# Optimization experiments

Measured on AMD Instinct MI355X. Metric: run time of the kernel, lower is better.

Reference implementation:

```python
import jax, jax.numpy as jnp
import numpy as np

B, D, OUT, K = 2048, 256, 256, 16


def setup_inputs() -> dict:
    key = jax.random.key(0)
    k1, k2, k3, k4 = jax.random.split(key, 4)
    x = jax.random.normal(k1, (B, D), dtype=jnp.float32)
    values = jax.random.uniform(k2, (OUT, D, K), dtype=jnp.float32, minval=-0.05, maxval=0.05)
    skip_w = jax.random.normal(k3, (OUT, D), dtype=jnp.float32) * (1.0 / np.sqrt(D).astype(np.float32))
    skip_b = jax.random.normal(k4, (OUT,), dtype=jnp.float32) * 0.01
    return {"x": x, "values": values, "skip_w": skip_w, "skip_b": skip_b}


def reference(x, values, skip_w, skip_b):
    # x: (B, D); values: (OUT, D, K); skip_w: (OUT, D); skip_b: (OUT,)
    num_knots = values.shape[-1]
    grid = jnp.linspace(-1.0, 1.0, num_knots)  # (K,)
    xc = jnp.clip(x, -1.0, 1.0)
    # torch.bucketize(x, grid) with right=False == searchsorted side='left'
    right = jnp.searchsorted(grid, xc, side='left')
    left = jnp.clip(right - 1, 0, num_knots - 2)  # (B, D)
    right = left + 1
    g0 = grid[left]
    g1 = grid[right]
    w = (xc - g0) / (g1 - g0 + 1e-12)  # (B, D)
    # Gather spline values per (sample, input-dim) knot bucket.
    vt = jnp.transpose(values, (1, 2, 0))  # (D, K, OUT)
    dim_idx = jnp.arange(xc.shape[1])[None, :]  # (1, D)
    v_left = vt[dim_idx, left]    # (B, D, OUT)
    v_right = vt[dim_idx, right]  # (B, D, OUT)
    # Linear interpolation + sum over input dims.
    y = jnp.sum((1.0 - w)[..., None] * v_left + w[..., None] * v_right, axis=1)  # (B, OUT)
    # Skip connection on the clamped input (torch reassigns x = clamp(x) first).
    return y + xc @ skip_w.T + skip_b
```

## Files before the change

kernel.cpp:

```cpp
#include <hip/hip_runtime.h>
#include <hip/hip_bf16.h>


namespace {
constexpr int Bsz  = 2048;
constexpr int Din  = 256;
constexpr int Dout = 256;
constexpr int Kn   = 16;
constexpr int KKNOT = Din * Kn;
constexpr int Ksp   = KKNOT + Din;
constexpr float INV_H = 7.5f;
constexpr float Hgrid = 2.0f / 15.0f;

constexpr int BM = 64, BN = 64, BK = 64;
constexpr int TOTSTEP = Ksp / BK;
constexpr int NSPLIT  = 4;
constexpr int STEPS   = TOTSTEP / NSPLIT;
constexpr int MT = Bsz / BM;
constexpr int NT = Dout / BN;
}

typedef __attribute__((ext_vector_type(8))) short shortx8;
typedef __attribute__((ext_vector_type(4))) float floatx4;
typedef __attribute__((address_space(3))) unsigned int lds_u32;
typedef __attribute__((address_space(1))) const unsigned int gbl_u32;

__device__ __forceinline__ unsigned int f2bf(float f) {
  __hip_bfloat16 h = __float2bfloat16(f);
  return (unsigned int)*reinterpret_cast<unsigned short*>(&h);
}

__global__ __launch_bounds__(256) void build_wt(
    const float* __restrict__ values, const float* __restrict__ skip_w,
    unsigned short* __restrict__ Wt) {
  const int c = blockIdx.x * 256 + threadIdx.x;
  const float* src;
  unsigned short* dst;
  if (c < KKNOT * Dout / 8) {
    const int o = c >> 9, i = c & 511;
    src = values + (size_t)c * 8;
    dst = Wt + (size_t)o * Ksp + i * 8;
  } else {
    const int c2 = c - KKNOT * Dout / 8;
    const int o = c2 >> 5, i = c2 & 31;
    src = skip_w + (size_t)c2 * 8;
    dst = Wt + (size_t)o * Ksp + KKNOT + i * 8;
  }
  const float4 v0 = *(const float4*)src;
  const float4 v1 = *(const float4*)(src + 4);
  *(uint4*)dst = make_uint4(f2bf(v0.x) | (f2bf(v0.y) << 16),
                            f2bf(v0.z) | (f2bf(v0.w) << 16),
                            f2bf(v1.x) | (f2bf(v1.y) << 16),
                            f2bf(v1.z) | (f2bf(v1.w) << 16));
}

__global__ __launch_bounds__(256) void kan_gemm(
    const float* __restrict__ x, const unsigned short* __restrict__ Wt,
    float* __restrict__ part) {
  __shared__ __align__(16) unsigned short As[BM][BK];
  __shared__ __align__(16) unsigned short Bs[BN][BK];

  const int tid = threadIdx.x;
  const int ks  = blockIdx.x % NSPLIT;
  const int nt  = (blockIdx.x / NSPLIT) % NT;
  const int mt  = blockIdx.x / (NSPLIT * NT);
  const int m0 = mt * BM, n0 = nt * BN;
  const int g0 = ks * STEPS, g1 = g0 + STEPS;

  const int row = tid >> 2;
  const int q   = tid & 3;
  const int b   = m0 + row;

  const int wave = tid >> 6, lane = tid & 63;
  const int wm = (wave & 1) * 32, wn = (wave >> 1) * 32;
  const int lrow = lane & 15, lq = lane >> 4;

  floatx4 acc[2][2] = {};

  for (int g = g0; g < g1; ++g) {
    __syncthreads();

    #pragma unroll
    for (int p = 0; p < 2; ++p) {
      const int c = tid + p * 256;
      const int n = c >> 3, kcs = c & 7;
      const int kc = kcs ^ (n & 7);
      const unsigned short* gsrc = Wt + (size_t)(n0 + n) * Ksp + g * 64 + kc * 8;
      unsigned int* l = (unsigned int*)(&Bs[0][0]) + c * 4;
      __builtin_amdgcn_global_load_lds((gbl_u32*)gsrc, (lds_u32*)l, 16, 0, 0);
    }

    unsigned int u[8];
    if (g < KKNOT / BK) {
      const float xr = x[(size_t)b * Din + 4 * g + q];
      const float t = (fminf(1.f, fmaxf(-1.f, xr)) + 1.f) * INV_H;
      #pragma unroll
      for (int i = 0; i < 8; ++i) {
        const float a0 = fmaxf(0.f, 1.f - fabsf(t - (float)(2 * i)));
        const float a1 = fmaxf(0.f, 1.f - fabsf(t - (float)(2 * i + 1)));
        u[i] = f2bf(a0) | (f2bf(a1) << 16);
      }
    } else {
      const int off = (g - KKNOT / BK) * 64 + q * 16;
      const float4* xq = (const float4*)(x + (size_t)b * Din + off);
      #pragma unroll
      for (int p = 0; p < 4; ++p) {
        const float4 v = xq[p];
        u[2 * p]     = f2bf(fminf(1.f, fmaxf(-1.f, v.x))) | (f2bf(fminf(1.f, fmaxf(-1.f, v.y))) << 16);
        u[2 * p + 1] = f2bf(fminf(1.f, fmaxf(-1.f, v.z))) | (f2bf(fminf(1.f, fmaxf(-1.f, v.w))) << 16);
      }
    }
    #pragma unroll
    for (int j = 0; j < 2; ++j) {
      const int slot = (2 * q + j) ^ (row & 7);
      *(uint4*)((char*)(&As[0][0]) + row * 128 + slot * 16) =
          make_uint4(u[4 * j], u[4 * j + 1], u[4 * j + 2], u[4 * j + 3]);
    }

    __syncthreads();

    shortx8 af[2][2], bfr[2][2];
    #pragma unroll
    for (int i = 0; i < 2; ++i) {
      const int r = wm + 16 * i + lrow;
      #pragma unroll
      for (int kk = 0; kk < 2; ++kk) {
        const int slot = (kk * 4 + lq) ^ (r & 7);
        af[i][kk] = *(const shortx8*)((const char*)(&As[0][0]) + r * 128 + slot * 16);
      }
    }
    #pragma unroll
    for (int j = 0; j < 2; ++j) {
      const int r = wn + 16 * j + lrow;
      #pragma unroll
      for (int kk = 0; kk < 2; ++kk) {
        const int slot = (kk * 4 + lq) ^ (r & 7);
        bfr[j][kk] = *(const shortx8*)((const char*)(&Bs[0][0]) + r * 128 + slot * 16);
      }
    }
    #pragma unroll
    for (int kk = 0; kk < 2; ++kk)
      #pragma unroll
      for (int i = 0; i < 2; ++i)
        #pragma unroll
        for (int j = 0; j < 2; ++j)
          acc[i][j] = __builtin_amdgcn_mfma_f32_16x16x32_bf16(af[i][kk], bfr[j][kk], acc[i][j], 0, 0, 0);
  }

  float* P = part + (size_t)ks * Bsz * Dout;
  #pragma unroll
  for (int i = 0; i < 2; ++i) {
    const int grow = m0 + wm + 16 * i + lq * 4;
    #pragma unroll
    for (int j = 0; j < 2; ++j) {
      const int gcol = n0 + wn + 16 * j + lrow;
      #pragma unroll
      for (int r = 0; r < 4; ++r)
        P[(size_t)(grow + r) * Dout + gcol] = acc[i][j][r];
    }
  }
}

__global__ __launch_bounds__(256) void kan_reduce(
    const float* __restrict__ part, const float* __restrict__ skip_b,
    float* __restrict__ out) {
  const int i = blockIdx.x * 256 + threadIdx.x;
  const int base = i * 4;
  const int o = base & (Dout - 1);
  float4 a = *(const float4*)(skip_b + o);
  #pragma unroll
  for (int s = 0; s < NSPLIT; ++s) {
    const float4 p = *(const float4*)(part + (size_t)s * Bsz * Dout + base);
    a.x += p.x; a.y += p.y; a.z += p.z; a.w += p.w;
  }
  *(float4*)(out + base) = a;
}

__device__ __forceinline__ void knot_interp(float xraw, float& xv, float& w, int& l) {
  xv = fminf(1.0f, fmaxf(-1.0f, xraw));
  float t = (xv + 1.0f) * INV_H;
  l = (int)ceilf(t) - 1;
  l = l < 0 ? 0 : (l > Kn - 2 ? Kn - 2 : l);
  float g0 = -1.0f + Hgrid * (float)l;
  w = (xv - g0) * INV_H;
}

__global__ __launch_bounds__(256) void prep_transpose(
    const float* __restrict__ values, const float* __restrict__ skip_w,
    float* __restrict__ vt, float* __restrict__ swt) {
  int idx = blockIdx.x * blockDim.x + threadIdx.x;
  if (idx < Din * Kn * Dout) {
    int k = idx & (Kn - 1);
    int d = (idx >> 4) & (Din - 1);
    int o = idx >> 12;
    vt[(d * Kn + k) * Dout + o] = values[idx];
  }
  if (idx < Dout * Din) {
    int d = idx & (Din - 1);
    int o = idx >> 8;
    swt[d * Dout + o] = skip_w[idx];
  }
}

__global__ __launch_bounds__(256) void kan_main(
    const float* __restrict__ x, const float* __restrict__ vt,
    const float* __restrict__ swt, const float* __restrict__ skip_b,
    float* __restrict__ out) {
  __shared__ float s_w[4][Din];
  __shared__ float s_x[4][Din];
  __shared__ int   s_l[4][Din];
  const int tid = threadIdx.x;
  const int b0  = blockIdx.x * 4;
  for (int i = tid; i < 4 * Din; i += 256) {
    int bb = i >> 8;
    int d  = i & (Din - 1);
    float xv, w; int l;
    knot_interp(x[(b0 + bb) * Din + d], xv, w, l);
    s_w[bb][d] = w; s_x[bb][d] = xv; s_l[bb][d] = l;
  }
  __syncthreads();
  const int g = tid >> 6, lane = tid & 63;
  const int o = lane << 2, b = b0 + g;
  float4 acc = make_float4(0.f, 0.f, 0.f, 0.f);
  for (int d = 0; d < Din; ++d) {
    const float w = s_w[g][d], xv = s_x[g][d];
    const int l = s_l[g][d];
    const float* base = vt + (d * Kn + l) * Dout + o;
    const float4 vl = *(const float4*)(base);
    const float4 vr = *(const float4*)(base + Dout);
    const float4 sw = *(const float4*)(swt + d * Dout + o);
    acc.x = fmaf(xv, sw.x, fmaf(w, vr.x - vl.x, acc.x + vl.x));
    acc.y = fmaf(xv, sw.y, fmaf(w, vr.y - vl.y, acc.y + vl.y));
    acc.z = fmaf(xv, sw.z, fmaf(w, vr.z - vl.z, acc.z + vl.z));
    acc.w = fmaf(xv, sw.w, fmaf(w, vr.w - vl.w, acc.w + vl.w));
  }
  const float4 bias = *(const float4*)(skip_b + o);
  acc.x += bias.x; acc.y += bias.y; acc.z += bias.z; acc.w += bias.w;
  *(float4*)(out + (size_t)b * Dout + o) = acc;
}

extern "C" void kernel_launch(void* const* d_in, const int* in_sizes, int n_in,
                              void* d_out, int out_size, void* d_ws, size_t ws_size,
                              hipStream_t stream) {
  (void)in_sizes; (void)n_in; (void)out_size;
  const float* x      = (const float*)d_in[0];
  const float* values = (const float*)d_in[1];
  const float* skip_w = (const float*)d_in[2];
  const float* skip_b = (const float*)d_in[3];
  float* out = (float*)d_out;

  const size_t wt_bytes   = (size_t)Dout * Ksp * sizeof(unsigned short);
  const size_t part_bytes = (size_t)NSPLIT * Bsz * Dout * sizeof(float);
  const size_t need_gemm  = wt_bytes + part_bytes;
  const size_t need_fb    = (size_t)(Din * Kn * Dout + Din * Dout) * sizeof(float);

  if (ws_size >= need_gemm) {
    unsigned short* Wt = (unsigned short*)d_ws;
    float* part = (float*)((char*)d_ws + wt_bytes);
    build_wt<<<(KKNOT * Dout / 8 + Din * Dout / 8 + 255) / 256, 256, 0, stream>>>(values, skip_w, Wt);
    kan_gemm<<<MT * NT * NSPLIT, 256, 0, stream>>>(x, Wt, part);
    kan_reduce<<<Bsz * Dout / 4 / 256, 256, 0, stream>>>(part, skip_b, out);
  } else if (ws_size >= need_fb) {
    float* vt  = (float*)d_ws;
    float* swt = vt + Din * Kn * Dout;
    prep_transpose<<<(Din * Kn * Dout + 255) / 256, 256, 0, stream>>>(values, skip_w, vt, swt);
    kan_main<<<Bsz / 4, 256, 0, stream>>>(x, vt, swt, skip_b, out);
  }
}
```

Before: 83.10 us.

## Precompute bf16 hat-basis activations and double-buffer GEMM tiles via registers

A new prep kernel materialises the bf16 hat-function basis and clamped x into a global activation matrix, fused with the weight conversion, so the GEMM no longer builds A tiles on the fly. The GEMM now prefetches the next A and B tiles into registers and stores them into double-buffered LDS, dropping one barrier per step. The K-split goes from 4 to 8 with 9 steps per split to raise block count. In exchange it writes and rereads roughly 17 MB of activations and doubles the partial-sum traffic for the reduce kernel.

```diff
diff --git a/kernel.cpp b/kernel.cpp
--- a/kernel.cpp
+++ b/kernel.cpp
@@ -14,110 +14,111 @@
 
 constexpr int BM = 64, BN = 64, BK = 64;
 constexpr int TOTSTEP = Ksp / BK;
-constexpr int NSPLIT  = 4;
-constexpr int STEPS   = TOTSTEP / NSPLIT;
+constexpr int NSPLIT  = 8;
+constexpr int SPS     = 9;
 constexpr int MT = Bsz / BM;
 constexpr int NT = Dout / BN;
 }
 
 typedef __attribute__((ext_vector_type(8))) short shortx8;
 typedef __attribute__((ext_vector_type(4))) float floatx4;
-typedef __attribute__((address_space(3))) unsigned int lds_u32;
-typedef __attribute__((address_space(1))) const unsigned int gbl_u32;
 
 __device__ __forceinline__ unsigned int f2bf(float f) {
   __hip_bfloat16 h = __float2bfloat16(f);
   return (unsigned int)*reinterpret_cast<unsigned short*>(&h);
 }
 
-__global__ __launch_bounds__(256) void build_wt(
-    const float* __restrict__ values, const float* __restrict__ skip_w,
+__global__ __launch_bounds__(256) void kan_prep(
+    const float* __restrict__ x, const float* __restrict__ values,
+    const float* __restrict__ skip_w, unsigned short* __restrict__ Abf,
     unsigned short* __restrict__ Wt) {
-  const int c = blockIdx.x * 256 + threadIdx.x;
-  const float* src;
-  unsigned short* dst;
-  if (c < KKNOT * Dout / 8) {
-    const int o = c >> 9, i = c & 511;
-    src = values + (size_t)c * 8;
-    dst = Wt + (size_t)o * Ksp + i * 8;
-  } else {
-    const int c2 = c - KKNOT * Dout / 8;
-    const int o = c2 >> 5, i = c2 & 31;
-    src = skip_w + (size_t)c2 * 8;
-    dst = Wt + (size_t)o * Ksp + KKNOT + i * 8;
-  }
-  const float4 v0 = *(const float4*)src;
-  const float4 v1 = *(const float4*)(src + 4);
-  *(uint4*)dst = make_uint4(f2bf(v0.x) | (f2bf(v0.y) << 16),
-                            f2bf(v0.z) | (f2bf(v0.w) << 16),
-                            f2bf(v1.x) | (f2bf(v1.y) << 16),
-                            f2bf(v1.z) | (f2bf(v1.w) << 16));
+  const int idx = blockIdx.x * 256 + threadIdx.x;
+  const int b = idx >> 8, d = idx & 255;
+
+  const float xr = x[idx];
+  const float xc = fminf(1.f, fmaxf(-1.f, xr));
+  const float t  = (xc + 1.f) * INV_H;
+  unsigned int u[8];
+  #pragma unroll
+  for (int i = 0; i < 8; ++i) {
+    const float a0 = fmaxf(0.f, 1.f - fabsf(t - (float)(2 * i)));
+    const float a1 = fmaxf(0.f, 1.f - fabsf(t - (float)(2 * i + 1)));
+    u[i] = f2bf(a0) | (f2bf(a1) << 16);
+  }
+  unsigned short* arow = Abf + (size_t)b * Ksp;
+  uint4* dst = (uint4*)(arow + d * 16);
+  dst[0] = make_uint4(u[0], u[1], u[2], u[3]);
+  dst[1] = make_uint4(u[4], u[5], u[6], u[7]);
+  arow[KKNOT + d] = (unsigned short)f2bf(xc);
+
+  if (idx < (KKNOT * Dout + Din * Dout) / 8) {
+    const float* src;
+    unsigned short* wdst;
+    if (idx < KKNOT * Dout / 8) {
+      const int o = idx >> 9, i = idx & 511;
+      src = values + (size_t)idx * 8;
+      wdst = Wt + (size_t)o * Ksp + i * 8;
+    } else {
+      const int c2 = idx - KKNOT * Dout / 8;
+      const int o = c2 >> 5, i = c2 & 31;
+      src = skip_w + (size_t)c2 * 8;
+      wdst = Wt + (size_t)o * Ksp + KKNOT + i * 8;
+    }
+    const float4 v0 = *(const float4*)src;
+    const float4 v1 = *(const float4*)(src + 4);
+    *(uint4*)wdst = make_uint4(f2bf(v0.x) | (f2bf(v0.y) << 16),
+                               f2bf(v0.z) | (f2bf(v0.w) << 16),
+                               f2bf(v1.x) | (f2bf(v1.y) << 16),
+                               f2bf(v1.z) | (f2bf(v1.w) << 16));
+  }
 }
 
 __global__ __launch_bounds__(256) void kan_gemm(
-    const float* __restrict__ x, const unsigned short* __restrict__ Wt,
+    const unsigned short* __restrict__ Abf, const unsigned short* __restrict__ Wt,
     float* __restrict__ part) {
-  __shared__ __align__(16) unsigned short As[BM][BK];
-  __shared__ __align__(16) unsigned short Bs[BN][BK];
+  __shared__ __align__(16) unsigned short As[2][BM][BK];
+  __shared__ __align__(16) unsigned short Bs[2][BN][BK];
 
   const int tid = threadIdx.x;
   const int ks  = blockIdx.x % NSPLIT;
   const int nt  = (blockIdx.x / NSPLIT) % NT;
   const int mt  = blockIdx.x / (NSPLIT * NT);
   const int m0 = mt * BM, n0 = nt * BN;
-  const int g0 = ks * STEPS, g1 = g0 + STEPS;
-
-  const int row = tid >> 2;
-  const int q   = tid & 3;
-  const int b   = m0 + row;
+  const int g0 = ks * SPS;
+  const int g1 = (g0 + SPS < TOTSTEP) ? g0 + SPS : TOTSTEP;
+
+  const unsigned short* ga[4];
+  #pragma unroll
+  for (int p = 0; p < 2; ++p) {
+    const int cc = tid + p * 256;
+    const int row = cc >> 3;
+    const int kc = (cc & 7) ^ (row & 7);
+    ga[p]     = Abf + (size_t)(m0 + row) * Ksp + kc * 8;
+    ga[p + 2] = Wt  + (size_t)(n0 + row) * Ksp + kc * 8;
+  }
 
   const int wave = tid >> 6, lane = tid & 63;
   const int wm = (wave & 1) * 32, wn = (wave >> 1) * 32;
   const int lrow = lane & 15, lq = lane >> 4;
 
   floatx4 acc[2][2] = {};
-
+  uint4 ra[4];
+
+  #pragma unroll
+  for (int p = 0; p < 4; ++p) ra[p] = *(const uint4*)(ga[p] + (size_t)g0 * 64);
+
+  int buf = 0;
   for (int g = g0; g < g1; ++g) {
+    *(uint4*)(&As[buf][0][0] + (size_t)tid * 8)         = ra[0];
+    *(uint4*)(&As[buf][0][0] + (size_t)(tid + 256) * 8) = ra[1];
+    *(uint4*)(&Bs[buf][0][0] + (size_t)tid * 8)         = ra[2];
+    *(uint4*)(&Bs[buf][0][0] + (size_t)(tid + 256) * 8) = ra[3];
     __syncthreads();
 
-    #pragma unroll
-    for (int p = 0; p < 2; ++p) {
-      const int c = tid + p * 256;
-      const int n = c >> 3, kcs = c & 7;
-      const int kc = kcs ^ (n & 7);
-      const unsigned short* gsrc = Wt + (size_t)(n0 + n) * Ksp + g * 64 + kc * 8;
-      unsigned int* l = (unsigned int*)(&Bs[0][0]) + c * 4;
-      __builtin_amdgcn_global_load_lds((gbl_u32*)gsrc, (lds_u32*)l, 16, 0, 0);
-    }
-
-    unsigned int u[8];
-    if (g < KKNOT / BK) {
-      const float xr = x[(size_t)b * Din + 4 * g + q];
-      const float t = (fminf(1.f, fmaxf(-1.f, xr)) + 1.f) * INV_H;
-      #pragma unroll
-      for (int i = 0; i < 8; ++i) {
-        const float a0 = fmaxf(0.f, 1.f - fabsf(t - (float)(2 * i)));
-        const float a1 = fmaxf(0.f, 1.f - fabsf(t - (float)(2 * i + 1)));
-        u[i] = f2bf(a0) | (f2bf(a1) << 16);
-      }
-    } else {
-      const int off = (g - KKNOT / BK) * 64 + q * 16;
-      const float4* xq = (const float4*)(x + (size_t)b * Din + off);
-      #pragma unroll
-      for (int p = 0; p < 4; ++p) {
-        const float4 v = xq[p];
-        u[2 * p]     = f2bf(fminf(1.f, fmaxf(-1.f, v.x))) | (f2bf(fminf(1.f, fmaxf(-1.f, v.y))) << 16);
-        u[2 * p + 1] = f2bf(fminf(1.f, fmaxf(-1.f, v.z))) | (f2bf(fminf(1.f, fmaxf(-1.f, v.w))) << 16);
-      }
-    }
-    #pragma unroll
-    for (int j = 0; j < 2; ++j) {
-      const int slot = (2 * q + j) ^ (row & 7);
-      *(uint4*)((char*)(&As[0][0]) + row * 128 + slot * 16) =
-          make_uint4(u[4 * j], u[4 * j + 1], u[4 * j + 2], u[4 * j + 3]);
-    }
-
-    __syncthreads();
+    if (g + 1 < g1) {
+      #pragma unroll
+      for (int p = 0; p < 4; ++p) ra[p] = *(const uint4*)(ga[p] + (size_t)(g + 1) * 64);
+    }
 
     shortx8 af[2][2], bfr[2][2];
     #pragma unroll
@@ -126,7 +127,7 @@
       #pragma unroll
       for (int kk = 0; kk < 2; ++kk) {
         const int slot = (kk * 4 + lq) ^ (r & 7);
-        af[i][kk] = *(const shortx8*)((const char*)(&As[0][0]) + r * 128 + slot * 16);
+        af[i][kk] = *(const shortx8*)(&As[buf][0][0] + r * 64 + slot * 8);
       }
     }
     #pragma unroll
@@ -135,7 +136,7 @@
       #pragma unroll
       for (int kk = 0; kk < 2; ++kk) {
         const int slot = (kk * 4 + lq) ^ (r & 7);
-        bfr[j][kk] = *(const shortx8*)((const char*)(&Bs[0][0]) + r * 128 + slot * 16);
+        bfr[j][kk] = *(const shortx8*)(&Bs[buf][0][0] + r * 64 + slot * 8);
       }
     }
     #pragma unroll
@@ -145,6 +146,8 @@
         #pragma unroll
         for (int j = 0; j < 2; ++j)
           acc[i][j] = __builtin_amdgcn_mfma_f32_16x16x32_bf16(af[i][kk], bfr[j][kk], acc[i][j], 0, 0, 0);
+
+    buf ^= 1;
   }
 
   float* P = part + (size_t)ks * Bsz * Dout;
@@ -249,16 +252,18 @@
   const float* skip_b = (const float*)d_in[3];
   float* out = (float*)d_out;
 
+  const size_t a_bytes    = (size_t)Bsz * Ksp * sizeof(unsigned short);
   const size_t wt_bytes   = (size_t)Dout * Ksp * sizeof(unsigned short);
   const size_t part_bytes = (size_t)NSPLIT * Bsz * Dout * sizeof(float);
-  const size_t need_gemm  = wt_bytes + part_bytes;
+  const size_t need_gemm  = a_bytes + wt_bytes + part_bytes;
   const size_t need_fb    = (size_t)(Din * Kn * Dout + Din * Dout) * sizeof(float);
 
   if (ws_size >= need_gemm) {
-    unsigned short* Wt = (unsigned short*)d_ws;
-    float* part = (float*)((char*)d_ws + wt_bytes);
-    build_wt<<<(KKNOT * Dout / 8 + Din * Dout / 8 + 255) / 256, 256, 0, stream>>>(values, skip_w, Wt);
-    kan_gemm<<<MT * NT * NSPLIT, 256, 0, stream>>>(x, Wt, part);
+    unsigned short* Abf = (unsigned short*)d_ws;
+    unsigned short* Wt  = (unsigned short*)((char*)d_ws + a_bytes);
+    float* part = (float*)((char*)d_ws + a_bytes + wt_bytes);
+    kan_prep<<<Bsz * Din / 256, 256, 0, stream>>>(x, values, skip_w, Abf, Wt);
+    kan_gemm<<<MT * NT * NSPLIT, 256, 0, stream>>>(Abf, Wt, part);
     kan_reduce<<<Bsz * Dout / 4 / 256, 256, 0, stream>>>(part, skip_b, out);
   } else if (ws_size >= need_fb) {
     float* vt  = (float*)d_ws;
```

Result: slower. 111.4 us (+34.0%).
